# Kernel optimization log

Measured on AMD Instinct MI355X. Metric: run time of the kernel, lower is better.

Reference implementation:

```python
import jax, jax.numpy as jnp
import numpy as np

C = 256
H = 4
D = C // H
SCALE = D ** -0.5
EPS = 1e-5


def _lin(x, W, b):
    # torch nn.Linear: y = x @ W.T + b, W: [out, in]
    return x @ W.T + b


def _heads(x):
    B, N, _ = x.shape
    return x.reshape(B, N, H, D).transpose(0, 2, 1, 3)  # [B,H,N,D]


def _merge(x):
    B, h, N, d = x.shape
    return x.transpose(0, 2, 1, 3).reshape(B, N, h * d)


def _attn(q, k, v):
    # q,k,v: [B,H,N,D]; materializes [B,H,N,N] scores like the original
    scores = jnp.einsum('bhnd,bhmd->bhnm', q, k) * SCALE
    p = jax.nn.softmax(scores, axis=-1)
    return jnp.einsum('bhnm,bhmd->bhnd', p, v)


def setup_inputs() -> dict:
    key = jax.random.key(0)
    ks = jax.random.split(key, 20)
    B, N = 4, 4096
    s = 0.02
    inp = {
        'f_freq': jax.random.normal(ks[0], (B, N, C), jnp.float32),
        'f_spat': jax.random.normal(ks[1], (B, N, C), jnp.float32),
        'Wqf': jax.random.normal(ks[2], (C, C), jnp.float32) * s,
        'bqf': jnp.zeros((C,), jnp.float32),
        'Wks': jax.random.normal(ks[3], (C, C), jnp.float32) * s,
        'bks': jnp.zeros((C,), jnp.float32),
        'Wvs': jax.random.normal(ks[4], (C, C), jnp.float32) * s,
        'bvs': jnp.zeros((C,), jnp.float32),
        'Wqs': jax.random.normal(ks[5], (C, C), jnp.float32) * s,
        'bqs': jnp.zeros((C,), jnp.float32),
        'Wkf': jax.random.normal(ks[6], (C, C), jnp.float32) * s,
        'bkf': jnp.zeros((C,), jnp.float32),
        'Wvf': jax.random.normal(ks[7], (C, C), jnp.float32) * s,
        'bvf': jnp.zeros((C,), jnp.float32),
        'Wp': jax.random.normal(ks[8], (C, 2 * C), jnp.float32) * s,
        'bp': jnp.zeros((C,), jnp.float32),
        'gamma': jnp.ones((C,), jnp.float32),
        'beta': jnp.zeros((C,), jnp.float32),
    }
    return inp


def reference(f_freq, f_spat, Wqf, bqf, Wks, bks, Wvs, bvs, Wqs, bqs,
              Wkf, bkf, Wvf, bvf, Wp, bp, gamma, beta):
    # direction 1: freq queries attend to spatial keys/values
    q_f = _heads(_lin(f_freq, Wqf, bqf))
    k_s = _heads(_lin(f_spat, Wks, bks))
    v_s = _heads(_lin(f_spat, Wvs, bvs))
    out_f2s = _merge(_attn(q_f, k_s, v_s))
    # direction 2: spatial queries attend to freq keys/values
    q_s = _heads(_lin(f_spat, Wqs, bqs))
    k_f = _heads(_lin(f_freq, Wkf, bkf))
    v_f = _heads(_lin(f_freq, Wvf, bvf))
    out_s2f = _merge(_attn(q_s, k_f, v_f))
    fused = _lin(jnp.concatenate([out_f2s, out_s2f], axis=-1), Wp, bp)
    # LayerNorm over last dim
    mu = jnp.mean(fused, axis=-1, keepdims=True)
    var = jnp.var(fused, axis=-1, keepdims=True)
    fused = (fused - mu) * jax.lax.rsqrt(var + EPS) * gamma + beta
    return fused
```

## Files before the change

kernel.cpp:

```cpp
#include <hip/hip_runtime.h>
#include <hip/hip_bf16.h>

typedef __attribute__((ext_vector_type(4))) float floatx4;
typedef __attribute__((ext_vector_type(8))) short shortx8;

#define MFMA(a, b, c) __builtin_amdgcn_mfma_f32_16x16x32_bf16(a, b, c, 0, 0, 0)

static constexpr int MTOT = 16384;
static constexpr int NSEQ = 4096;
static constexpr int CD = 256;
static constexpr float SEXP = 0.18033688011112042f;

__device__ __forceinline__ unsigned short f2bf(float f) {
  unsigned int u = __float_as_uint(f);
  u += 0x7fffu + ((u >> 16) & 1u);
  return (unsigned short)(u >> 16);
}

__device__ __forceinline__ shortx8 ld8(const unsigned short* p) {
  return *reinterpret_cast<const shortx8*>(p);
}

__device__ __forceinline__ void gl_lds16(const unsigned short* g, unsigned short* l) {
  __builtin_amdgcn_global_load_lds(
      (const __attribute__((address_space(1))) unsigned int*)g,
      (__attribute__((address_space(3))) unsigned int*)l, 16, 0, 0);
}

__global__ __launch_bounds__(256) void cast_x(const float* __restrict__ s0,
                                              const float* __restrict__ s1,
                                              unsigned short* __restrict__ d0,
                                              unsigned short* __restrict__ d1) {
  const float* src = blockIdx.y ? s1 : s0;
  unsigned short* dst = blockIdx.y ? d1 : d0;
  int i = (blockIdx.x * 256 + threadIdx.x) * 4;
  float4 v = *reinterpret_cast<const float4*>(src + i);
  ushort4 o;
  o.x = f2bf(v.x); o.y = f2bf(v.y); o.z = f2bf(v.z); o.w = f2bf(v.w);
  *reinterpret_cast<ushort4*>(dst + i) = o;
}

struct WSrc { const float* p[8]; };
__global__ __launch_bounds__(256) void cast_w(WSrc srcs, unsigned short* __restrict__ dst) {
  const int j = blockIdx.y;
  const float* src = srcs.p[j];
  int i = (blockIdx.x * 256 + threadIdx.x) * 4;
  float4 v = *reinterpret_cast<const float4*>(src + i);
  ushort4 o;
  o.x = f2bf(v.x); o.y = f2bf(v.y); o.z = f2bf(v.z); o.w = f2bf(v.w);
  *reinterpret_cast<ushort4*>(dst + j * 65536 + i) = o;
}

struct BiasPtrs { const float* p[6]; };

__global__ __launch_bounds__(256, 4) void qkv_gemm(const unsigned short* __restrict__ Xf,
                                                   const unsigned short* __restrict__ Xs,
                                                   const unsigned short* __restrict__ W6,
                                                   BiasPtrs bias6,
                                                   unsigned short* __restrict__ Yout) {
  __shared__ unsigned short smem[16384];
  const int j = blockIdx.y >> 1;
  const int o128 = (blockIdx.y & 1) * 128;
  const unsigned short* X = ((14 >> j) & 1) ? Xs : Xf;
  const unsigned short* W = W6 + j * 65536;
  const float* bias = bias6.p[j];
  const float sc = (j == 0 || j == 3) ? SEXP : 1.0f;
  unsigned short* Y = Yout + (size_t)j * MTOT * CD;

  const int wave = threadIdx.x >> 6, lane = threadIdx.x & 63;
  const int col = lane & 15, quad = lane >> 4;
  const int m0 = blockIdx.x * 128;
  const int mq = (wave & 1) * 64, oq = (wave >> 1) * 64;

  const int rA = lane >> 2, cA = lane & 3;
  const unsigned short* pA = X + (size_t)(m0 + wave * 32 + rA) * CD + cA * 8;
  const unsigned short* pB = W + (size_t)(o128 + wave * 32 + rA) * CD + cA * 8;
  unsigned short* lA = &smem[wave * 1024];
  unsigned short* lB = &smem[8192 + wave * 1024];

#define QSTAGE(BUF)                                   \
  do {                                                \
    gl_lds16(pA, lA + (BUF) * 4096);                  \
    gl_lds16(pA + 16 * CD, lA + (BUF) * 4096 + 512);  \
    gl_lds16(pB, lB + (BUF) * 4096);                  \
    gl_lds16(pB + 16 * CD, lB + (BUF) * 4096 + 512);  \
    pA += 32;                                         \
    pB += 32;                                         \
  } while (0)

  floatx4 acc[4][4];
  for (int mt = 0; mt < 4; ++mt)
    for (int f = 0; f < 4; ++f) acc[mt][f] = floatx4{0.f, 0.f, 0.f, 0.f};

  QSTAGE(0);
  __syncthreads();

  int buf = 0;
  for (int ks = 0; ks < 8; ++ks, buf ^= 1) {
    if (ks + 1 < 8) QSTAGE(buf ^ 1);
    shortx8 a[4], b[4];
    for (int mt = 0; mt < 4; ++mt)
      a[mt] = ld8(&smem[buf * 4096 + (mq + mt * 16 + col) * 32 + quad * 8]);
    for (int f = 0; f < 4; ++f)
      b[f] = ld8(&smem[8192 + buf * 4096 + (oq + f * 16 + col) * 32 + quad * 8]);
    for (int mt = 0; mt < 4; ++mt)
      for (int f = 0; f < 4; ++f)
        acc[mt][f] = MFMA(a[mt], b[f], acc[mt][f]);
    __syncthreads();
  }
#undef QSTAGE

  for (int mt = 0; mt < 4; ++mt)
    for (int f = 0; f < 4; ++f) {
      const int oc = o128 + oq + f * 16 + col;
      const float bv = bias[oc];
      for (int r = 0; r < 4; ++r)
        Y[(size_t)(m0 + mq + mt * 16 + quad * 4 + r) * CD + oc] =
            f2bf((acc[mt][f][r] + bv) * sc);
    }
}

__global__ __launch_bounds__(256) void vtrans(const unsigned short* __restrict__ qkv,
                                              unsigned short* __restrict__ Vt) {
  __shared__ unsigned short tile[64][65];
  const int pb = blockIdx.y;
  const int dir = pb >> 4, b = (pb >> 2) & 3, h = pb & 3;
  const size_t SZ = (size_t)MTOT * CD;
  const unsigned short* V = qkv + (size_t)dir * 3 * SZ + 2 * SZ;
  const int n0 = blockIdx.x * 64;
  const int t = threadIdx.x;
  const int dcol = t & 63, nrow = t >> 6;
  for (int nn = 0; nn < 64; nn += 4)
    tile[nn + nrow][dcol] = V[(size_t)(b * NSEQ + n0 + nn + nrow) * CD + h * 64 + dcol];
  __syncthreads();
  const int ncol = t & 63, drow = t >> 6;
  unsigned short* dst = Vt + (size_t)pb * 64 * NSEQ;
  for (int dd = 0; dd < 64; dd += 4)
    dst[(size_t)(dd + drow) * NSEQ + n0 + ncol] = tile[ncol][dd + drow];
}

__global__ __launch_bounds__(256, 4) void attn_kernel(const unsigned short* __restrict__ qkv,
                                                      const unsigned short* __restrict__ Vt,
                                                      unsigned short* __restrict__ Oout) {
  __shared__ unsigned short smem[16384];
  const size_t SZ = (size_t)MTOT * CD;
  const int pb = blockIdx.y;
  const int dir = pb >> 4, b = (pb >> 2) & 3, h4 = pb & 3;
  const unsigned short* Q = qkv + (size_t)dir * 3 * SZ;
  const unsigned short* K = Q + SZ;
  const unsigned short* VT = Vt + (size_t)pb * 64 * NSEQ;
  unsigned short* O = Oout + (size_t)dir * SZ;

  const int wave = threadIdx.x >> 6, lane = threadIdx.x & 63;
  const int col = lane & 15, quad = lane >> 4;
  const int rowbase = b * NSEQ;
  const int cb = h4 * 64;
  const int q0 = blockIdx.x * 128 + wave * 32;

  shortx8 qf[2][2];
  for (int mt = 0; mt < 2; ++mt)
    for (int c = 0; c < 2; ++c)
      qf[mt][c] = ld8(Q + (size_t)(rowbase + q0 + mt * 16 + col) * CD + cb + c * 32 + quad * 8);

  floatx4 oacc[2][4];
  floatx4 lacc[2];
  for (int mt = 0; mt < 2; ++mt) {
    for (int d = 0; d < 4; ++d) oacc[mt][d] = floatx4{0.f, 0.f, 0.f, 0.f};
    lacc[mt] = floatx4{0.f, 0.f, 0.f, 0.f};
  }
  shortx8 ones;
  for (int i = 0; i < 8; ++i) ones[i] = (short)0x3F80;

  const int gp = 8 * (col >> 2) + (col & 3);
  const int swb = 2 * (col & 3);

  int kbase[2][2], vbase[2][4];
  for (int t = 0; t < 2; ++t)
    for (int c = 0; c < 2; ++c)
      kbase[t][c] = (gp + 4 * t) * 64 + ((c * 4 + quad + swb) & 7) * 8;
  for (int h = 0; h < 2; ++h)
    for (int db = 0; db < 4; ++db)
      vbase[h][db] = (db * 16 + col) * 64 + ((h * 4 + quad + swb) & 7) * 8;

  const int r8 = lane >> 3;
  const int cg = (lane - 2 * r8) & 7;

  const unsigned short* pk = K + (size_t)(rowbase + wave * 16 + r8) * CD + cb + cg * 8;
  const unsigned short* pv = VT + (size_t)(wave * 16 + r8) * NSEQ + cg * 8;
  unsigned short* lk = &smem[wave * 1024];
  unsigned short* lv = &smem[8192 + wave * 1024];

#define STAGE(BUF)                                  \
  do {                                              \
    gl_lds16(pk, lk + (BUF) * 4096);                \
    gl_lds16(pk + 8 * CD, lk + (BUF) * 4096 + 512); \
    gl_lds16(pv, lv + (BUF) * 4096);                \
    gl_lds16(pv + 8 * NSEQ, lv + (BUF) * 4096 + 512);\
    pk += 64 * CD;                                  \
    pv += 64;                                       \
  } while (0)

  STAGE(0);
  __syncthreads();

  int buf = 0;
  for (int kt = 0; kt < NSEQ; kt += 64, buf ^= 1) {
    if (kt + 64 < NSEQ) STAGE(buf ^ 1);

    for (int h = 0; h < 2; ++h) {
      shortx8 kf[2][2], vf[4];
      const int kb = buf * 4096 + h * 2048;
      for (int t = 0; t < 2; ++t)
        for (int c = 0; c < 2; ++c) kf[t][c] = ld8(&smem[kb + kbase[t][c]]);
      const int vb = 8192 + buf * 4096;
      for (int db = 0; db < 4; ++db) vf[db] = ld8(&smem[vb + vbase[h][db]]);

      for (int mt = 0; mt < 2; ++mt) {
        floatx4 z = floatx4{0.f, 0.f, 0.f, 0.f};
        floatx4 st0 = MFMA(kf[0][0], qf[mt][0], z);
        st0 = MFMA(kf[0][1], qf[mt][1], st0);
        floatx4 st1 = MFMA(kf[1][0], qf[mt][0], z);
        st1 = MFMA(kf[1][1], qf[mt][1], st1);
        float p[8];
        for (int r = 0; r < 4; ++r) {
          p[r]     = __builtin_amdgcn_exp2f(st0[r]);
          p[4 + r] = __builtin_amdgcn_exp2f(st1[r]);
        }
        union { shortx8 s8; unsigned int u[4]; } pu;
        for (int w = 0; w < 4; ++w)
          pu.u[w] = __builtin_amdgcn_perm(__float_as_uint(p[2 * w + 1]),
                                          __float_as_uint(p[2 * w]), 0x07060302u);
        lacc[mt] = MFMA(ones, pu.s8, lacc[mt]);
        for (int db = 0; db < 4; ++db)
          oacc[mt][db] = MFMA(vf[db], pu.s8, oacc[mt][db]);
      }
    }
    __syncthreads();
  }
#undef STAGE

  for (int mt = 0; mt < 2; ++mt) {
    const float inv = 1.0f / lacc[mt][0];
    for (int db = 0; db < 4; ++db) {
      ushort4 o4;
      o4.x = f2bf(oacc[mt][db][0] * inv);
      o4.y = f2bf(oacc[mt][db][1] * inv);
      o4.z = f2bf(oacc[mt][db][2] * inv);
      o4.w = f2bf(oacc[mt][db][3] * inv);
      *reinterpret_cast<ushort4*>(
          O + (size_t)(rowbase + q0 + mt * 16 + col) * CD + cb + db * 16 + quad * 4) = o4;
    }
  }
}

__global__ __launch_bounds__(256) void final_ln(const unsigned short* __restrict__ O1,
                                                const unsigned short* __restrict__ O2,
                                                const unsigned short* __restrict__ Wp,
                                                const float* __restrict__ bp,
                                                const float* __restrict__ gamma,
                                                const float* __restrict__ beta,
                                                float* __restrict__ out) {
  __shared__ float ssum[4][32], ssq[4][32];
  const int wave = threadIdx.x >> 6, lane = threadIdx.x & 63;
  const int col = lane & 15, quad = lane >> 4;
  const int m0 = blockIdx.x * 32;
  const int o0 = wave * 64;

  floatx4 acc[2][4];
  for (int mt = 0; mt < 2; ++mt)
    for (int f = 0; f < 4; ++f) acc[mt][f] = floatx4{0.f, 0.f, 0.f, 0.f};

  for (int kk = 0; kk < 16; ++kk) {
    const unsigned short* src = (kk < 8) ? O1 : O2;
    const int k0 = (kk & 7) * 32;
    shortx8 a[2], bb[4];
    for (int mt = 0; mt < 2; ++mt)
      a[mt] = ld8(src + (size_t)(m0 + mt * 16 + col) * CD + k0 + quad * 8);
    for (int f = 0; f < 4; ++f)
      bb[f] = ld8(Wp + (size_t)(o0 + f * 16 + col) * 512 + kk * 32 + quad * 8);
    for (int mt = 0; mt < 2; ++mt)
      for (int f = 0; f < 4; ++f)
        acc[mt][f] = MFMA(a[mt], bb[f], acc[mt][f]);
  }

  float vals[2][4][4];
  for (int mt = 0; mt < 2; ++mt)
    for (int f = 0; f < 4; ++f) {
      const float bv = bp[o0 + f * 16 + col];
      for (int r = 0; r < 4; ++r) vals[mt][f][r] = acc[mt][f][r] + bv;
    }

  for (int mt = 0; mt < 2; ++mt)
    for (int r = 0; r < 4; ++r) {
      float s = 0.f, q = 0.f;
      for (int f = 0; f < 4; ++f) { float v = vals[mt][f][r]; s += v; q += v * v; }
      for (int d = 1; d < 16; d <<= 1) { s += __shfl_xor(s, d); q += __shfl_xor(q, d); }
      if (col == 0) {
        ssum[wave][mt * 16 + quad * 4 + r] = s;
        ssq[wave][mt * 16 + quad * 4 + r] = q;
      }
    }
  __syncthreads();
  for (int mt = 0; mt < 2; ++mt)
    for (int r = 0; r < 4; ++r) {
      const int rl = mt * 16 + quad * 4 + r;
      const float S = ssum[0][rl] + ssum[1][rl] + ssum[2][rl] + ssum[3][rl];
      const float Qs = ssq[0][rl] + ssq[1][rl] + ssq[2][rl] + ssq[3][rl];
      const float mean = S * (1.0f / 256.0f);
      const float var = Qs * (1.0f / 256.0f) - mean * mean;
      const float rs = rsqrtf(var + 1e-5f);
      for (int f = 0; f < 4; ++f) {
        const int oc = o0 + f * 16 + col;
        out[(size_t)(m0 + rl) * CD + oc] = (vals[mt][f][r] - mean) * rs * gamma[oc] + beta[oc];
      }
    }
}

extern "C" void kernel_launch(void* const* d_in, const int* in_sizes, int n_in,
                              void* d_out, int out_size, void* d_ws, size_t ws_size,
                              hipStream_t stream) {
  const float* f_freq = (const float*)d_in[0];
  const float* f_spat = (const float*)d_in[1];
  const float* Wqf = (const float*)d_in[2];  const float* bqf = (const float*)d_in[3];
  const float* Wks = (const float*)d_in[4];  const float* bks = (const float*)d_in[5];
  const float* Wvs = (const float*)d_in[6];  const float* bvs = (const float*)d_in[7];
  const float* Wqs = (const float*)d_in[8];  const float* bqs = (const float*)d_in[9];
  const float* Wkf = (const float*)d_in[10]; const float* bkf = (const float*)d_in[11];
  const float* Wvf = (const float*)d_in[12]; const float* bvf = (const float*)d_in[13];
  const float* Wp  = (const float*)d_in[14]; const float* bp  = (const float*)d_in[15];
  const float* gamma = (const float*)d_in[16];
  const float* beta  = (const float*)d_in[17];
  float* out = (float*)d_out;

  const size_t SZ = (size_t)MTOT * CD;
  unsigned short* Xf  = (unsigned short*)d_ws;
  unsigned short* Xs  = Xf + SZ;
  unsigned short* W6  = Xs + SZ;
  unsigned short* WpB = W6 + 6 * 65536;
  unsigned short* QKV = WpB + 131072;
  unsigned short* O1  = QKV + 6 * SZ;
  unsigned short* O2  = O1 + SZ;
  unsigned short* Vt  = Xf;

  cast_x<<<dim3(4096, 2), 256, 0, stream>>>(f_freq, f_spat, Xf, Xs);
  WSrc ws8 = {{Wqf, Wks, Wvs, Wqs, Wkf, Wvf, Wp, Wp + 65536}};
  cast_w<<<dim3(64, 8), 256, 0, stream>>>(ws8, W6);

  BiasPtrs bias6 = {{bqf, bks, bvs, bqs, bkf, bvf}};
  qkv_gemm<<<dim3(128, 12), 256, 0, stream>>>(Xf, Xs, W6, bias6, QKV);

  vtrans<<<dim3(64, 32), 256, 0, stream>>>(QKV, Vt);

  attn_kernel<<<dim3(32, 32), 256, 0, stream>>>(QKV, Vt, O1);

  final_ln<<<512, 256, 0, stream>>>(O1, O2, WpB, bp, gamma, beta, out);
}
```

Baseline: 308.3 us.

## Fuse V transpose into QKV GEMM epilogue and merge cast kernels

The QKV GEMM now computes V projections with swapped MFMA operands and writes V directly in the per-head transposed [d][n] layout, which removes the separate vtrans kernel and its extra read/write pass over V. The two cast kernels are merged into a single launch. The attention loop is manually unrolled by two so buffer indices are compile-time constants. The transposed V epilogue writes strided 2-byte stores per row, which may be less coalesced than the original store pattern.

```diff
diff --git a/kernel.cpp b/kernel.cpp
--- a/kernel.cpp
+++ b/kernel.cpp
@@ -27,28 +27,32 @@
       (__attribute__((address_space(3))) unsigned int*)l, 16, 0, 0);
 }
 
-__global__ __launch_bounds__(256) void cast_x(const float* __restrict__ s0,
-                                              const float* __restrict__ s1,
-                                              unsigned short* __restrict__ d0,
-                                              unsigned short* __restrict__ d1) {
-  const float* src = blockIdx.y ? s1 : s0;
-  unsigned short* dst = blockIdx.y ? d1 : d0;
-  int i = (blockIdx.x * 256 + threadIdx.x) * 4;
-  float4 v = *reinterpret_cast<const float4*>(src + i);
+struct CastArgs { const float* src[10]; };
+
+__global__ __launch_bounds__(256) void cast_all(CastArgs a,
+                                                unsigned short* __restrict__ xf,
+                                                unsigned short* __restrict__ xs,
+                                                unsigned short* __restrict__ wcat) {
+  const int bx = blockIdx.x;
+  const float* s;
+  unsigned short* d;
+  int off;
+  if (bx < 8192) {
+    const int which = bx >> 12;
+    s = a.src[which];
+    d = which ? xs : xf;
+    off = (bx & 4095) * 1024 + threadIdx.x * 4;
+  } else {
+    const int w = bx - 8192;
+    const int j = w >> 6;
+    s = a.src[2 + j];
+    d = wcat + j * 65536;
+    off = (w & 63) * 1024 + threadIdx.x * 4;
+  }
+  float4 v = *reinterpret_cast<const float4*>(s + off);
   ushort4 o;
   o.x = f2bf(v.x); o.y = f2bf(v.y); o.z = f2bf(v.z); o.w = f2bf(v.w);
-  *reinterpret_cast<ushort4*>(dst + i) = o;
-}
-
-struct WSrc { const float* p[8]; };
-__global__ __launch_bounds__(256) void cast_w(WSrc srcs, unsigned short* __restrict__ dst) {
-  const int j = blockIdx.y;
-  const float* src = srcs.p[j];
-  int i = (blockIdx.x * 256 + threadIdx.x) * 4;
-  float4 v = *reinterpret_cast<const float4*>(src + i);
-  ushort4 o;
-  o.x = f2bf(v.x); o.y = f2bf(v.y); o.z = f2bf(v.z); o.w = f2bf(v.w);
-  *reinterpret_cast<ushort4*>(dst + j * 65536 + i) = o;
+  *reinterpret_cast<ushort4*>(d + off) = o;
 }
 
 struct BiasPtrs { const float* p[6]; };
@@ -61,6 +65,7 @@
   __shared__ unsigned short smem[16384];
   const int j = blockIdx.y >> 1;
   const int o128 = (blockIdx.y & 1) * 128;
+  const bool isV = (j == 2) || (j == 5);
   const unsigned short* X = ((14 >> j) & 1) ? Xs : Xf;
   const unsigned short* W = W6 + j * 65536;
   const float* bias = bias6.p[j];
@@ -103,44 +108,45 @@
       a[mt] = ld8(&smem[buf * 4096 + (mq + mt * 16 + col) * 32 + quad * 8]);
     for (int f = 0; f < 4; ++f)
       b[f] = ld8(&smem[8192 + buf * 4096 + (oq + f * 16 + col) * 32 + quad * 8]);
+    if (!isV) {
+      for (int mt = 0; mt < 4; ++mt)
+        for (int f = 0; f < 4; ++f)
+          acc[mt][f] = MFMA(a[mt], b[f], acc[mt][f]);
+    } else {
+      for (int mt = 0; mt < 4; ++mt)
+        for (int f = 0; f < 4; ++f)
+          acc[mt][f] = MFMA(b[mt], a[f], acc[mt][f]);
+    }
+    __syncthreads();
+  }
+#undef QSTAGE
+
+  if (!isV) {
     for (int mt = 0; mt < 4; ++mt)
-      for (int f = 0; f < 4; ++f)
-        acc[mt][f] = MFMA(a[mt], b[f], acc[mt][f]);
-    __syncthreads();
-  }
-#undef QSTAGE
-
-  for (int mt = 0; mt < 4; ++mt)
-    for (int f = 0; f < 4; ++f) {
-      const int oc = o128 + oq + f * 16 + col;
-      const float bv = bias[oc];
-      for (int r = 0; r < 4; ++r)
-        Y[(size_t)(m0 + mq + mt * 16 + quad * 4 + r) * CD + oc] =
-            f2bf((acc[mt][f][r] + bv) * sc);
-    }
-}
-
-__global__ __launch_bounds__(256) void vtrans(const unsigned short* __restrict__ qkv,
-                                              unsigned short* __restrict__ Vt) {
-  __shared__ unsigned short tile[64][65];
-  const int pb = blockIdx.y;
-  const int dir = pb >> 4, b = (pb >> 2) & 3, h = pb & 3;
-  const size_t SZ = (size_t)MTOT * CD;
-  const unsigned short* V = qkv + (size_t)dir * 3 * SZ + 2 * SZ;
-  const int n0 = blockIdx.x * 64;
-  const int t = threadIdx.x;
-  const int dcol = t & 63, nrow = t >> 6;
-  for (int nn = 0; nn < 64; nn += 4)
-    tile[nn + nrow][dcol] = V[(size_t)(b * NSEQ + n0 + nn + nrow) * CD + h * 64 + dcol];
-  __syncthreads();
-  const int ncol = t & 63, drow = t >> 6;
-  unsigned short* dst = Vt + (size_t)pb * 64 * NSEQ;
-  for (int dd = 0; dd < 64; dd += 4)
-    dst[(size_t)(dd + drow) * NSEQ + n0 + ncol] = tile[ncol][dd + drow];
+      for (int f = 0; f < 4; ++f) {
+        const int oc = o128 + oq + f * 16 + col;
+        const float bv = bias[oc];
+        for (int r = 0; r < 4; ++r)
+          Y[(size_t)(m0 + mq + mt * 16 + quad * 4 + r) * CD + oc] =
+              f2bf((acc[mt][f][r] + bv) * sc);
+      }
+  } else {
+    const int bloc = m0 >> 12;
+    const int nbase = (m0 & 4095) + mq;
+    for (int mt = 0; mt < 4; ++mt)
+      for (int r = 0; r < 4; ++r) {
+        const int wg = o128 + oq + mt * 16 + quad * 4 + r;
+        const int h = wg >> 6, dloc = wg & 63;
+        const float bv = bias[wg];
+        unsigned short* dst =
+            Y + (size_t)(bloc * 4 + h) * 64 * NSEQ + (size_t)dloc * NSEQ + nbase;
+        for (int f = 0; f < 4; ++f)
+          dst[f * 16 + col] = f2bf(acc[mt][f][r] + bv);
+      }
+  }
 }
 
 __global__ __launch_bounds__(256, 4) void attn_kernel(const unsigned short* __restrict__ qkv,
-                                                      const unsigned short* __restrict__ Vt,
                                                       unsigned short* __restrict__ Oout) {
   __shared__ unsigned short smem[16384];
   const size_t SZ = (size_t)MTOT * CD;
@@ -148,7 +154,7 @@
   const int dir = pb >> 4, b = (pb >> 2) & 3, h4 = pb & 3;
   const unsigned short* Q = qkv + (size_t)dir * 3 * SZ;
   const unsigned short* K = Q + SZ;
-  const unsigned short* VT = Vt + (size_t)pb * 64 * NSEQ;
+  const unsigned short* VT = K + SZ + (size_t)(b * 4 + h4) * 64 * NSEQ;
   unsigned short* O = Oout + (size_t)dir * SZ;
 
   const int wave = threadIdx.x >> 6, lane = threadIdx.x & 63;
@@ -200,44 +206,48 @@
     pv += 64;                                       \
   } while (0)
 
+#define PROCESS(BUF)                                                                   \
+  for (int h = 0; h < 2; ++h) {                                                        \
+    shortx8 kf[2][2], vf[4];                                                           \
+    for (int t = 0; t < 2; ++t)                                                        \
+      for (int c = 0; c < 2; ++c)                                                      \
+        kf[t][c] = ld8(&smem[(BUF) * 4096 + h * 2048 + kbase[t][c]]);                  \
+    for (int db = 0; db < 4; ++db)                                                     \
+      vf[db] = ld8(&smem[8192 + (BUF) * 4096 + vbase[h][db]]);                         \
+    for (int mt = 0; mt < 2; ++mt) {                                                   \
+      floatx4 z = floatx4{0.f, 0.f, 0.f, 0.f};                                         \
+      floatx4 st0 = MFMA(kf[0][0], qf[mt][0], z);                                      \
+      st0 = MFMA(kf[0][1], qf[mt][1], st0);                                            \
+      floatx4 st1 = MFMA(kf[1][0], qf[mt][0], z);                                      \
+      st1 = MFMA(kf[1][1], qf[mt][1], st1);                                            \
+      float p[8];                                                                      \
+      for (int r = 0; r < 4; ++r) {                                                    \
+        p[r]     = __builtin_amdgcn_exp2f(st0[r]);                                     \
+        p[4 + r] = __builtin_amdgcn_exp2f(st1[r]);                                     \
+      }                                                                                \
+      union { shortx8 s8; unsigned int u[4]; } pu;                                     \
+      for (int w = 0; w < 4; ++w)                                                      \
+        pu.u[w] = __builtin_amdgcn_perm(__float_as_uint(p[2 * w + 1]),                 \
+                                        __float_as_uint(p[2 * w]), 0x07060302u);       \
+      lacc[mt] = MFMA(ones, pu.s8, lacc[mt]);                                          \
+      for (int db = 0; db < 4; ++db)                                                   \
+        oacc[mt][db] = MFMA(vf[db], pu.s8, oacc[mt][db]);                              \
+    }                                                                                  \
+  }
+
   STAGE(0);
   __syncthreads();
 
-  int buf = 0;
-  for (int kt = 0; kt < NSEQ; kt += 64, buf ^= 1) {
-    if (kt + 64 < NSEQ) STAGE(buf ^ 1);
-
-    for (int h = 0; h < 2; ++h) {
-      shortx8 kf[2][2], vf[4];
-      const int kb = buf * 4096 + h * 2048;
-      for (int t = 0; t < 2; ++t)
-        for (int c = 0; c < 2; ++c) kf[t][c] = ld8(&smem[kb + kbase[t][c]]);
-      const int vb = 8192 + buf * 4096;
-      for (int db = 0; db < 4; ++db) vf[db] = ld8(&smem[vb + vbase[h][db]]);
-
-      for (int mt = 0; mt < 2; ++mt) {
-        floatx4 z = floatx4{0.f, 0.f, 0.f, 0.f};
-        floatx4 st0 = MFMA(kf[0][0], qf[mt][0], z);
-        st0 = MFMA(kf[0][1], qf[mt][1], st0);
-        floatx4 st1 = MFMA(kf[1][0], qf[mt][0], z);
-        st1 = MFMA(kf[1][1], qf[mt][1], st1);
-        float p[8];
-        for (int r = 0; r < 4; ++r) {
-          p[r]     = __builtin_amdgcn_exp2f(st0[r]);
-          p[4 + r] = __builtin_amdgcn_exp2f(st1[r]);
-        }
-        union { shortx8 s8; unsigned int u[4]; } pu;
-        for (int w = 0; w < 4; ++w)
-          pu.u[w] = __builtin_amdgcn_perm(__float_as_uint(p[2 * w + 1]),
-                                          __float_as_uint(p[2 * w]), 0x07060302u);
-        lacc[mt] = MFMA(ones, pu.s8, lacc[mt]);
-        for (int db = 0; db < 4; ++db)
-          oacc[mt][db] = MFMA(vf[db], pu.s8, oacc[mt][db]);
-      }
-    }
+  for (int kt = 0; kt < NSEQ; kt += 128) {
+    if (kt + 64 < NSEQ) STAGE(1);
+    PROCESS(0)
     __syncthreads();
+    if (kt + 128 < NSEQ) STAGE(0);
+    PROCESS(1)
+    __syncthreads();
   }
 #undef STAGE
+#undef PROCESS
 
   for (int mt = 0; mt < 2; ++mt) {
     const float inv = 1.0f / lacc[mt][0];
@@ -340,18 +350,14 @@
   unsigned short* QKV = WpB + 131072;
   unsigned short* O1  = QKV + 6 * SZ;
   unsigned short* O2  = O1 + SZ;
-  unsigned short* Vt  = Xf;
-
-  cast_x<<<dim3(4096, 2), 256, 0, stream>>>(f_freq, f_spat, Xf, Xs);
-  WSrc ws8 = {{Wqf, Wks, Wvs, Wqs, Wkf, Wvf, Wp, Wp + 65536}};
-  cast_w<<<dim3(64, 8), 256, 0, stream>>>(ws8, W6);
+
+  CastArgs ca = {{f_freq, f_spat, Wqf, Wks, Wvs, Wqs, Wkf, Wvf, Wp, Wp + 65536}};
+  cast_all<<<8704, 256, 0, stream>>>(ca, Xf, Xs, W6);
 
   BiasPtrs bias6 = {{bqf, bks, bvs, bqs, bkf, bvf}};
   qkv_gemm<<<dim3(128, 12), 256, 0, stream>>>(Xf, Xs, W6, bias6, QKV);
 
-  vtrans<<<dim3(64, 32), 256, 0, stream>>>(QKV, Vt);
-
-  attn_kernel<<<dim3(32, 32), 256, 0, stream>>>(QKV, Vt, O1);
+  attn_kernel<<<dim3(32, 32), 256, 0, stream>>>(QKV, O1);
 
   final_ln<<<512, 256, 0, stream>>>(O1, O2, WpB, bp, gamma, beta, out);
 }
```

Measured after the change: 382.3 us. +24.0%, slower.
